# Optimization experiments

Measured on AMD Instinct MI355X. Metric: run time of the kernel, lower is better.

Reference implementation:

```python
import jax, jax.numpy as jnp
import numpy as np


def setup_inputs() -> dict:
    key = jax.random.key(0)
    k1, k2, k3, k4 = jax.random.split(key, 4)
    Q, S, L, F, H = 32, 25, 64, 256, 64
    qs = jax.random.normal(k1, (Q, L, F), dtype=jnp.float32)
    hs = jax.random.normal(k2, (S, L, F), dtype=jnp.float32)
    # nn.Linear(feature_size, hidden_size): weight [H, F], bias [H]
    W = jax.random.normal(k3, (H, F), dtype=jnp.float32) * (1.0 / np.sqrt(F))
    b = jax.random.normal(k4, (H,), dtype=jnp.float32) * 0.01
    return {"qs": qs, "hs": hs, "W": W, "b": b}


def reference(qs, hs, W, b):
    # Project once instead of materializing the repeated 5D tensors before Linear.
    # Wq: [Q, L, H], Wh: [S, L, H]
    Wq = jnp.einsum("qlf,hf->qlh", qs, W) + b
    Wh = jnp.einsum("slf,hf->slh", hs, W) + b
    # score[q,s,i,j] = sum_h tanh(Wq[q,i,h] * Wh[s,j,h])  -- non-decomposable,
    # so the broadcasted [Q,S,L,L,H] tanh is the faithful (and dominant) compute.
    scores = jnp.sum(
        jnp.tanh(Wq[:, None, :, None, :] * Wh[None, :, None, :, :]), axis=-1
    )  # [Q, S, L, L]
    att = jax.nn.softmax(scores, axis=3)  # softmax over support sequence dim j
    # weighted sum of support states: hs_rep[q,s,i,j,:] = hs[s,j,:]
    out = jnp.einsum("qsij,sjf->qsif", att, hs)  # [Q, S, L, F]
    return out
```

## Files before the change

### kernel.cpp

```cpp
#include <hip/hip_runtime.h>


#define NQ 32
#define NS 25
#define NL 64
#define NF 256
#define NH 64

#define K2LOG2E 2.8853900817779268f
#define C_LOG2E 1.4426950408889634f

typedef __attribute__((ext_vector_type(8))) short bf16x8;
typedef __attribute__((ext_vector_type(4))) float f32x4;

__device__ inline unsigned short f2bf(float x) {
    union { float f; unsigned int u; } v; v.f = x;
    unsigned int r = v.u + 0x7fffu + ((v.u >> 16) & 1u);
    return (unsigned short)(r >> 16);
}

__device__ inline void cvt_hilo(float4 a, float4 b, bf16x8* hi, bf16x8* lo) {
    float x[8] = {a.x, a.y, a.z, a.w, b.x, b.y, b.z, b.w};
    bf16x8 h8, l8;
#pragma unroll
    for (int i = 0; i < 8; ++i) {
        union { float f; unsigned int u; } v; v.f = x[i];
        unsigned short hh = (unsigned short)(v.u >> 16);
        h8[i] = (short)hh;
        union { unsigned int u; float f; } hf; hf.u = (unsigned int)hh << 16;
        union { float f; unsigned int u; } rv; rv.f = x[i] - hf.f;
        l8[i] = (short)(unsigned short)(rv.u >> 16);
    }
    *hi = h8; *lo = l8;
}

#define PROJ_BLOCKS 114
__global__ __launch_bounds__(256) void prep_kernel(
    const float* __restrict__ qs, const float* __restrict__ hs,
    const float* __restrict__ W, const float* __restrict__ b,
    float* __restrict__ Wqs, float* __restrict__ Whs,
    unsigned short* __restrict__ hsT)
{
    __shared__ unsigned short T[64 * 72];
    const int t = threadIdx.x;
    const int bid = blockIdx.x;

    if (bid < PROJ_BLOCKS) {
        const int w = t >> 6, lane = t & 63;
        const int m15 = lane & 15, quad = lane >> 4;
        const int r0 = bid * 32 + (w & 1) * 16;
        const int h0 = (w >> 1) * 32;
        const bool is_q = (r0 < 2048);
        const float* Xrow = is_q ? (qs + (size_t)(r0 + m15) * NF)
                                 : (hs + (size_t)(r0 - 2048 + m15) * NF);
        f32x4 acc[2] = {(f32x4){0.f,0.f,0.f,0.f}, (f32x4){0.f,0.f,0.f,0.f}};

#pragma unroll 2
        for (int kk = 0; kk < 8; ++kk) {
            const int f0 = kk * 32 + quad * 8;
            bf16x8 xhi, xlo;
            cvt_hilo(*(const float4*)(Xrow + f0), *(const float4*)(Xrow + f0 + 4),
                     &xhi, &xlo);
#pragma unroll
            for (int nt = 0; nt < 2; ++nt) {
                const float* Wrow = W + (size_t)(h0 + nt * 16 + m15) * NF + f0;
                bf16x8 whi, wlo;
                cvt_hilo(*(const float4*)(Wrow), *(const float4*)(Wrow + 4),
                         &whi, &wlo);
                acc[nt] = __builtin_amdgcn_mfma_f32_16x16x32_bf16(xhi, whi, acc[nt], 0, 0, 0);
                acc[nt] = __builtin_amdgcn_mfma_f32_16x16x32_bf16(xhi, wlo, acc[nt], 0, 0, 0);
                acc[nt] = __builtin_amdgcn_mfma_f32_16x16x32_bf16(xlo, whi, acc[nt], 0, 0, 0);
            }
        }
#pragma unroll
        for (int nt = 0; nt < 2; ++nt) {
            const int h = h0 + nt * 16 + m15;
            const float bias = b[h];
#pragma unroll
            for (int r = 0; r < 4; ++r) {
                const int row = r0 + quad * 4 + r;
                const float v = acc[nt][r] + bias;
                if (is_q) Wqs[(size_t)row * NH + h] = v * K2LOG2E;
                else      Whs[(size_t)(row - 2048) * NH + h] = v;
            }
        }
    } else {
        const int b2 = bid - PROJ_BLOCKS;
        const int s = b2 >> 2;
        const int f0 = (b2 & 3) * 64;
        const float4* h4p = (const float4*)(hs + (size_t)s * NL * NF);
#pragma unroll
        for (int u = 0; u < 4; ++u) {
            int idx = t + 256 * u;
            int j = idx >> 4, fq = idx & 15;
            float4 v = h4p[j * 64 + (f0 >> 2) + fq];
            T[(4 * fq + 0) * 72 + j] = f2bf(v.x);
            T[(4 * fq + 1) * 72 + j] = f2bf(v.y);
            T[(4 * fq + 2) * 72 + j] = f2bf(v.z);
            T[(4 * fq + 3) * 72 + j] = f2bf(v.w);
        }
        __syncthreads();
#pragma unroll
        for (int u = 0; u < 2; ++u) {
            int idx = t + 256 * u;
            int fl = idx >> 3, jg = idx & 7;
            uint4 v = *(const uint4*)&T[fl * 72 + jg * 8];
            *(uint4*)&hsT[(size_t)(s * 256 + f0 + fl) * 64 + jg * 8] = v;
        }
    }
}

#define AS 68
#define B_OFF 2176
#define SCS 65
#define ATT_BYTE 8704
#define SMEMF 6528

__global__ __launch_bounds__(256, 6) void attn_kernel(
    const float* __restrict__ Wqs, const float* __restrict__ Whs,
    const unsigned short* __restrict__ hsT, float* __restrict__ out)
{
    __shared__ float smem[SMEMF];
    const int t = threadIdx.x;
    const int bid = blockIdx.x;
    const int half = bid & 1;
    const int s = (bid >> 1) % NS;
    const int q = bid / (2 * NS);

    {
        const float4* a4 = (const float4*)(Wqs + ((size_t)q * NL + half * 32) * NH);
        const float4* b4 = (const float4*)(Whs + (size_t)s * NL * NH);
#pragma unroll
        for (int u = 0; u < 2; ++u) {
            int idx = t + 256 * u;
            int i = idx >> 4, g = idx & 15;
            *(float4*)&smem[i * AS + 4 * g] = a4[idx];
        }
#pragma unroll
        for (int u = 0; u < 4; ++u) {
            int idx = t + 256 * u;
            int j = idx >> 4, g = idx & 15;
            *(float4*)&smem[B_OFF + j * AS + 4 * g] = b4[idx];
        }
    }
    __syncthreads();

    const int i0 = (t >> 4) * 2;
    const int jn = t & 15;
    float sum[2][4] = {{0.f, 0.f, 0.f, 0.f}, {0.f, 0.f, 0.f, 0.f}};

#pragma unroll 2
    for (int h4 = 0; h4 < 16; ++h4) {
        float4 av[2], bv[4];
        av[0] = *(const float4*)&smem[i0 * AS + 4 * h4];
        av[1] = *(const float4*)&smem[(i0 + 1) * AS + 4 * h4];
#pragma unroll
        for (int jj = 0; jj < 4; ++jj)
            bv[jj] = *(const float4*)&smem[B_OFF + (jn + 16 * jj) * AS + 4 * h4];
#pragma unroll
        for (int ii = 0; ii < 2; ++ii) {
#pragma unroll
            for (int jj = 0; jj < 4; ++jj) {
                float e0 = __builtin_amdgcn_exp2f(fminf(av[ii].x * bv[jj].x, 18.f));
                float e1 = __builtin_amdgcn_exp2f(fminf(av[ii].y * bv[jj].y, 18.f));
                float e2 = __builtin_amdgcn_exp2f(fminf(av[ii].z * bv[jj].z, 18.f));
                float e3 = __builtin_amdgcn_exp2f(fminf(av[ii].w * bv[jj].w, 18.f));
                float s01 = e0 + e1, s23 = e2 + e3;
                float d01 = fmaf(e0, e1, s01) + 1.f;
                float d23 = fmaf(e2, e3, s23) + 1.f;
                float num = fmaf(s01 + 2.f, d23, (s23 + 2.f) * d01);
                sum[ii][jj] = fmaf(num, __builtin_amdgcn_rcpf(d01 * d23), sum[ii][jj]);
            }
        }
    }
    __syncthreads();

#pragma unroll
    for (int ii = 0; ii < 2; ++ii)
#pragma unroll
        for (int jj = 0; jj < 4; ++jj)
            smem[(i0 + ii) * SCS + jn + 16 * jj] = -2.f * sum[ii][jj];
    __syncthreads();

    {
        const int i = t >> 3, c = t & 7;
        const float* row = &smem[i * SCS + c * 8];
        float v[8];
        float m = -1e30f;
#pragma unroll
        for (int k = 0; k < 8; ++k) { v[k] = row[k]; m = fmaxf(m, v[k]); }
        m = fmaxf(m, __shfl_xor(m, 1));
        m = fmaxf(m, __shfl_xor(m, 2));
        m = fmaxf(m, __shfl_xor(m, 4));
        float d = 0.f;
#pragma unroll
        for (int k = 0; k < 8; ++k) {
            float p = __builtin_amdgcn_exp2f((v[k] - m) * C_LOG2E);
            v[k] = p; d += p;
        }
        d += __shfl_xor(d, 1);
        d += __shfl_xor(d, 2);
        d += __shfl_xor(d, 4);
        const float inv = __builtin_amdgcn_rcpf(d);
        unsigned int w0 = f2bf(v[0] * inv) | ((unsigned int)f2bf(v[1] * inv) << 16);
        unsigned int w1 = f2bf(v[2] * inv) | ((unsigned int)f2bf(v[3] * inv) << 16);
        unsigned int w2 = f2bf(v[4] * inv) | ((unsigned int)f2bf(v[5] * inv) << 16);
        unsigned int w3 = f2bf(v[6] * inv) | ((unsigned int)f2bf(v[7] * inv) << 16);
        *(uint4*)((char*)smem + ATT_BYTE + i * 144 + c * 16) = make_uint4(w0, w1, w2, w3);
    }
    __syncthreads();

    const int lane = t & 63;
    const int wv = t >> 6;
    const int m15 = lane & 15;
    const int quad = lane >> 4;

    bf16x8 afr[2][2];
#pragma unroll
    for (int m = 0; m < 2; ++m)
#pragma unroll
        for (int k = 0; k < 2; ++k)
            afr[m][k] = *(const bf16x8*)((const char*)smem + ATT_BYTE
                          + (m * 16 + m15) * 144 + k * 64 + quad * 16);

    const unsigned short* hsTs = hsT + (size_t)s * NF * NL;
    f32x4 acc[2][4];
#pragma unroll
    for (int m = 0; m < 2; ++m)
#pragma unroll
        for (int n = 0; n < 4; ++n) acc[m][n] = (f32x4){0.f, 0.f, 0.f, 0.f};

#pragma unroll
    for (int k = 0; k < 2; ++k) {
        bf16x8 bfr[4];
#pragma unroll
        for (int n = 0; n < 4; ++n)
            bfr[n] = *(const bf16x8*)(hsTs
                        + (size_t)((wv * 4 + n) * 16 + m15) * 64 + k * 32 + quad * 8);
#pragma unroll
        for (int m = 0; m < 2; ++m)
#pragma unroll
            for (int n = 0; n < 4; ++n)
                acc[m][n] = __builtin_amdgcn_mfma_f32_16x16x32_bf16(
                    afr[m][k], bfr[n], acc[m][n], 0, 0, 0);
    }

    const size_t obase = ((size_t)(q * NS + s) * NL + half * 32) * NF;
#pragma unroll
    for (int m = 0; m < 2; ++m)
#pragma unroll
        for (int n = 0; n < 4; ++n)
#pragma unroll
            for (int r = 0; r < 4; ++r)
                out[obase + (size_t)(m * 16 + quad * 4 + r) * NF
                    + (wv * 4 + n) * 16 + m15] = acc[m][n][r];
}

extern "C" void kernel_launch(void* const* d_in, const int* in_sizes, int n_in,
                              void* d_out, int out_size, void* d_ws, size_t ws_size,
                              hipStream_t stream) {
    const float* qs = (const float*)d_in[0];
    const float* hs = (const float*)d_in[1];
    const float* W  = (const float*)d_in[2];
    const float* b  = (const float*)d_in[3];
    float* out = (float*)d_out;

    float* Wqs = (float*)d_ws;
    float* Whs = Wqs + NQ * NL * NH;
    unsigned short* hsT = (unsigned short*)(Whs + NS * NL * NH);

    prep_kernel<<<PROJ_BLOCKS + NS * 4, 256, 0, stream>>>(qs, hs, W, b, Wqs, Whs, hsT);
    attn_kernel<<<NQ * NS * 2, 256, 0, stream>>>(Wqs, Whs, hsT, out);
}
```

Before: 122.6 us.

## Split attention blocks into 16-row query tiles and softmax in registers

Each block now handles 16 query rows instead of 32, which doubles the grid to 3200 blocks, shrinks shared memory and raises launch bounds occupancy to 7. Each thread computes one row against four columns, so the softmax runs directly on register scores with 16-lane shuffles and skips the score round-trip through shared memory and one barrier. The cost is that each block reloads the full Wh tile and hsT slice for half as many rows, and each loaded av value is reused less.

```diff
diff --git a/kernel.cpp b/kernel.cpp
--- a/kernel.cpp
+++ b/kernel.cpp
@@ -111,30 +111,26 @@
 }
 
 #define AS 68
-#define B_OFF 2176
-#define SCS 65
-#define ATT_BYTE 8704
-#define SMEMF 6528
-
-__global__ __launch_bounds__(256, 6) void attn_kernel(
+#define B_OFF 1088
+#define SMEMF 5440
+
+__global__ __launch_bounds__(256, 7) void attn_kernel(
     const float* __restrict__ Wqs, const float* __restrict__ Whs,
     const unsigned short* __restrict__ hsT, float* __restrict__ out)
 {
     __shared__ float smem[SMEMF];
     const int t = threadIdx.x;
     const int bid = blockIdx.x;
-    const int half = bid & 1;
-    const int s = (bid >> 1) % NS;
-    const int q = bid / (2 * NS);
+    const int qt = bid & 3;
+    const int s = (bid >> 2) % NS;
+    const int q = bid / (4 * NS);
 
     {
-        const float4* a4 = (const float4*)(Wqs + ((size_t)q * NL + half * 32) * NH);
+        const float4* a4 = (const float4*)(Wqs + ((size_t)q * NL + qt * 16) * NH);
         const float4* b4 = (const float4*)(Whs + (size_t)s * NL * NH);
-#pragma unroll
-        for (int u = 0; u < 2; ++u) {
-            int idx = t + 256 * u;
-            int i = idx >> 4, g = idx & 15;
-            *(float4*)&smem[i * AS + 4 * g] = a4[idx];
+        {
+            int i = t >> 4, g = t & 15;
+            *(float4*)&smem[i * AS + 4 * g] = a4[t];
         }
 #pragma unroll
         for (int u = 0; u < 4; ++u) {
@@ -145,68 +141,57 @@
     }
     __syncthreads();
 
-    const int i0 = (t >> 4) * 2;
+    const int irow = t >> 4;
     const int jn = t & 15;
-    float sum[2][4] = {{0.f, 0.f, 0.f, 0.f}, {0.f, 0.f, 0.f, 0.f}};
-
-#pragma unroll 2
+    float sum[4] = {0.f, 0.f, 0.f, 0.f};
+
+#pragma unroll 4
     for (int h4 = 0; h4 < 16; ++h4) {
-        float4 av[2], bv[4];
-        av[0] = *(const float4*)&smem[i0 * AS + 4 * h4];
-        av[1] = *(const float4*)&smem[(i0 + 1) * AS + 4 * h4];
+        float4 av = *(const float4*)&smem[irow * AS + 4 * h4];
+        float4 bv[4];
 #pragma unroll
         for (int jj = 0; jj < 4; ++jj)
             bv[jj] = *(const float4*)&smem[B_OFF + (jn + 16 * jj) * AS + 4 * h4];
 #pragma unroll
-        for (int ii = 0; ii < 2; ++ii) {
-#pragma unroll
-            for (int jj = 0; jj < 4; ++jj) {
-                float e0 = __builtin_amdgcn_exp2f(fminf(av[ii].x * bv[jj].x, 18.f));
-                float e1 = __builtin_amdgcn_exp2f(fminf(av[ii].y * bv[jj].y, 18.f));
-                float e2 = __builtin_amdgcn_exp2f(fminf(av[ii].z * bv[jj].z, 18.f));
-                float e3 = __builtin_amdgcn_exp2f(fminf(av[ii].w * bv[jj].w, 18.f));
-                float s01 = e0 + e1, s23 = e2 + e3;
-                float d01 = fmaf(e0, e1, s01) + 1.f;
-                float d23 = fmaf(e2, e3, s23) + 1.f;
-                float num = fmaf(s01 + 2.f, d23, (s23 + 2.f) * d01);
-                sum[ii][jj] = fmaf(num, __builtin_amdgcn_rcpf(d01 * d23), sum[ii][jj]);
-            }
+        for (int jj = 0; jj < 4; ++jj) {
+            float e0 = __builtin_amdgcn_exp2f(fminf(av.x * bv[jj].x, 18.f));
+            float e1 = __builtin_amdgcn_exp2f(fminf(av.y * bv[jj].y, 18.f));
+            float e2 = __builtin_amdgcn_exp2f(fminf(av.z * bv[jj].z, 18.f));
+            float e3 = __builtin_amdgcn_exp2f(fminf(av.w * bv[jj].w, 18.f));
+            float s01 = e0 + e1, s23 = e2 + e3;
+            float d01 = fmaf(e0, e1, s01) + 1.f;
+            float d23 = fmaf(e2, e3, s23) + 1.f;
+            float num = fmaf(s01 + 2.f, d23, (s23 + 2.f) * d01);
+            sum[jj] = fmaf(num, __builtin_amdgcn_rcpf(d01 * d23), sum[jj]);
         }
     }
     __syncthreads();
 
-#pragma unroll
-    for (int ii = 0; ii < 2; ++ii)
-#pragma unroll
-        for (int jj = 0; jj < 4; ++jj)
-            smem[(i0 + ii) * SCS + jn + 16 * jj] = -2.f * sum[ii][jj];
-    __syncthreads();
-
     {
-        const int i = t >> 3, c = t & 7;
-        const float* row = &smem[i * SCS + c * 8];
-        float v[8];
-        float m = -1e30f;
-#pragma unroll
-        for (int k = 0; k < 8; ++k) { v[k] = row[k]; m = fmaxf(m, v[k]); }
+        float sc[4];
+#pragma unroll
+        for (int jj = 0; jj < 4; ++jj) sc[jj] = -2.f * sum[jj];
+        float m = fmaxf(fmaxf(sc[0], sc[1]), fmaxf(sc[2], sc[3]));
         m = fmaxf(m, __shfl_xor(m, 1));
         m = fmaxf(m, __shfl_xor(m, 2));
         m = fmaxf(m, __shfl_xor(m, 4));
+        m = fmaxf(m, __shfl_xor(m, 8));
+        float p[4];
         float d = 0.f;
 #pragma unroll
-        for (int k = 0; k < 8; ++k) {
-            float p = __builtin_amdgcn_exp2f((v[k] - m) * C_LOG2E);
-            v[k] = p; d += p;
+        for (int jj = 0; jj < 4; ++jj) {
+            p[jj] = __builtin_amdgcn_exp2f((sc[jj] - m) * C_LOG2E);
+            d += p[jj];
         }
         d += __shfl_xor(d, 1);
         d += __shfl_xor(d, 2);
         d += __shfl_xor(d, 4);
+        d += __shfl_xor(d, 8);
         const float inv = __builtin_amdgcn_rcpf(d);
-        unsigned int w0 = f2bf(v[0] * inv) | ((unsigned int)f2bf(v[1] * inv) << 16);
-        unsigned int w1 = f2bf(v[2] * inv) | ((unsigned int)f2bf(v[3] * inv) << 16);
-        unsigned int w2 = f2bf(v[4] * inv) | ((unsigned int)f2bf(v[5] * inv) << 16);
-        unsigned int w3 = f2bf(v[6] * inv) | ((unsigned int)f2bf(v[7] * inv) << 16);
-        *(uint4*)((char*)smem + ATT_BYTE + i * 144 + c * 16) = make_uint4(w0, w1, w2, w3);
+        unsigned short* att = (unsigned short*)smem;
+#pragma unroll
+        for (int jj = 0; jj < 4; ++jj)
+            att[irow * 72 + jn + 16 * jj] = f2bf(p[jj] * inv);
     }
     __syncthreads();
 
@@ -215,20 +200,15 @@
     const int m15 = lane & 15;
     const int quad = lane >> 4;
 
-    bf16x8 afr[2][2];
-#pragma unroll
-    for (int m = 0; m < 2; ++m)
-#pragma unroll
-        for (int k = 0; k < 2; ++k)
-            afr[m][k] = *(const bf16x8*)((const char*)smem + ATT_BYTE
-                          + (m * 16 + m15) * 144 + k * 64 + quad * 16);
+    bf16x8 afr[2];
+#pragma unroll
+    for (int k = 0; k < 2; ++k)
+        afr[k] = *(const bf16x8*)((const char*)smem + m15 * 144 + k * 64 + quad * 16);
 
     const unsigned short* hsTs = hsT + (size_t)s * NF * NL;
-    f32x4 acc[2][4];
-#pragma unroll
-    for (int m = 0; m < 2; ++m)
-#pragma unroll
-        for (int n = 0; n < 4; ++n) acc[m][n] = (f32x4){0.f, 0.f, 0.f, 0.f};
+    f32x4 acc[4];
+#pragma unroll
+    for (int n = 0; n < 4; ++n) acc[n] = (f32x4){0.f, 0.f, 0.f, 0.f};
 
 #pragma unroll
     for (int k = 0; k < 2; ++k) {
@@ -238,22 +218,16 @@
             bfr[n] = *(const bf16x8*)(hsTs
                         + (size_t)((wv * 4 + n) * 16 + m15) * 64 + k * 32 + quad * 8);
 #pragma unroll
-        for (int m = 0; m < 2; ++m)
-#pragma unroll
-            for (int n = 0; n < 4; ++n)
-                acc[m][n] = __builtin_amdgcn_mfma_f32_16x16x32_bf16(
-                    afr[m][k], bfr[n], acc[m][n], 0, 0, 0);
-    }
-
-    const size_t obase = ((size_t)(q * NS + s) * NL + half * 32) * NF;
-#pragma unroll
-    for (int m = 0; m < 2; ++m)
-#pragma unroll
         for (int n = 0; n < 4; ++n)
-#pragma unroll
-            for (int r = 0; r < 4; ++r)
-                out[obase + (size_t)(m * 16 + quad * 4 + r) * NF
-                    + (wv * 4 + n) * 16 + m15] = acc[m][n][r];
+            acc[n] = __builtin_amdgcn_mfma_f32_16x16x32_bf16(afr[k], bfr[n], acc[n], 0, 0, 0);
+    }
+
+    const size_t obase = ((size_t)(q * NS + s) * NL + qt * 16) * NF;
+#pragma unroll
+    for (int n = 0; n < 4; ++n)
+#pragma unroll
+        for (int r = 0; r < 4; ++r)
+            out[obase + (size_t)(quad * 4 + r) * NF + (wv * 4 + n) * 16 + m15] = acc[n][r];
 }
 
 extern "C" void kernel_launch(void* const* d_in, const int* in_sizes, int n_in,
@@ -270,5 +244,5 @@
     unsigned short* hsT = (unsigned short*)(Whs + NS * NL * NH);
 
     prep_kernel<<<PROJ_BLOCKS + NS * 4, 256, 0, stream>>>(qs, hs, W, b, Wqs, Whs, hsT);
-    attn_kernel<<<NQ * NS * 2, 256, 0, stream>>>(Wqs, Whs, hsT, out);
-}
+    attn_kernel<<<NQ * NS * 4, 256, 0, stream>>>(Wqs, Whs, hsT, out);
+}
```

Result: faster. 119.5 us (-2.5%).
